# Performance work log

Measured on AMD Instinct MI355X. Metric: run time of the kernel, lower is better.

## Reference

```python
import jax, jax.numpy as jnp
import numpy as np

B, C, W, H = 2, 64, 96, 96  # N = W*H = 9216 spatial positions


def conv1x1(x, w, b):
    # x: (B, Cin, W, H), w: (Cout, Cin), b: (Cout,) -> (B, Cout, W, H)
    return jnp.einsum('bchw,oc->bohw', x, w) + b[None, :, None, None]


def setup_inputs() -> dict:
    key = jax.random.key(0)
    ks = jax.random.split(key, 4)
    c8 = C // 8
    s = 0.05  # small weight scale keeps softmax logits in a sane range
    return {
        'x': jax.random.normal(ks[0], (B, C, W, H), jnp.float32),
        'wq': jax.random.normal(ks[1], (c8, C), jnp.float32) * s,
        'bq': jnp.zeros((c8,), jnp.float32),
        'wk': jax.random.normal(ks[2], (c8, C), jnp.float32) * s,
        'bk': jnp.zeros((c8,), jnp.float32),
        'wv': jax.random.normal(ks[3], (C, C), jnp.float32) * s,
        'bv': jnp.zeros((C,), jnp.float32),
        'gamma': jnp.full((1,), 0.5, jnp.float32),
    }


def reference(x, wq, bq, wk, bk, wv, bv, gamma):
    b, c, w, h = x.shape
    n = w * h
    q = conv1x1(x, wq, bq).reshape(b, -1, n)   # (B, C//8, N)
    k = conv1x1(x, wk, bk).reshape(b, -1, n)   # (B, C//8, N)
    v = conv1x1(x, wv, bv).reshape(b, c, n)    # (B, C, N)
    energy = jnp.einsum('bci,bcj->bij', q, k)  # (B, N, N)
    attn = jax.nn.softmax(energy, axis=-1)
    # torch.bmm(v, attn): out[b,c,i] = sum_j v[b,c,j] * attn[b,j,i]
    out = jnp.einsum('bcj,bji->bci', v, attn).reshape(b, c, w, h)
    return gamma * out + x
```

## Files before the change

kernel.cpp:

```cpp
#include <hip/hip_runtime.h>

using half2v  = __attribute__((ext_vector_type(2))) _Float16;
using half4   = __attribute__((ext_vector_type(4))) _Float16;
using half8   = __attribute__((ext_vector_type(8))) _Float16;
using floatx4 = __attribute__((ext_vector_type(4))) float;

constexpr int BATCH = 2;
constexpr int NPOS  = 96 * 96;
constexpr int NT    = NPOS / 16;
constexpr int NST   = NPOS / 32;

#define EXP2(x) __builtin_amdgcn_exp2f(x)
#define MFMA16(A, B, C) __builtin_amdgcn_mfma_f32_16x16x16f16(A, B, C, 0, 0, 0)
#define MFMA32(A, B, C) __builtin_amdgcn_mfma_f32_16x16x32_f16(A, B, C, 0, 0, 0)

__device__ inline half8 p8_of(floatx4 e0, floatx4 e1) {
    half2v a0 = __builtin_bit_cast(half2v,
        __builtin_amdgcn_cvt_pkrtz(EXP2(e0[0]), EXP2(e0[1])));
    half2v a1 = __builtin_bit_cast(half2v,
        __builtin_amdgcn_cvt_pkrtz(EXP2(e0[2]), EXP2(e0[3])));
    half2v a2 = __builtin_bit_cast(half2v,
        __builtin_amdgcn_cvt_pkrtz(EXP2(e1[0]), EXP2(e1[1])));
    half2v a3 = __builtin_bit_cast(half2v,
        __builtin_amdgcn_cvt_pkrtz(EXP2(e1[2]), EXP2(e1[3])));
    half8 p = {a0[0], a0[1], a1[0], a1[1], a2[0], a2[1], a3[0], a3[1]};
    return p;
}

__global__ __launch_bounds__(256) void qkv_kernel(
    const float* __restrict__ x,
    const float* __restrict__ wq, const float* __restrict__ bq,
    const float* __restrict__ wk, const float* __restrict__ bk,
    const float* __restrict__ wv, const float* __restrict__ bv,
    _Float16* __restrict__ Qf, _Float16* __restrict__ Kf,
    _Float16* __restrict__ Vf)
{
    __shared__ float W[80][64];
    __shared__ float bias[80];
    __shared__ float qs[32][9];
    __shared__ float ks[32][9];
    __shared__ _Float16 vs[32][72];
    const int tid = threadIdx.x;
    for (int idx = tid; idx < 80 * 64; idx += 256) {
        int o = idx >> 6, c = idx & 63;
        float w;
        if (o < 8)       w = wq[o * 64 + c];
        else if (o < 16) w = wk[(o - 8) * 64 + c];
        else             w = wv[(o - 16) * 64 + c];
        W[o][c] = w;
    }
    if (tid < 80) {
        float bb;
        if (tid < 8)       bb = bq[tid];
        else if (tid < 16) bb = bk[tid - 8];
        else               bb = bv[tid - 16];
        bias[tid] = bb;
    }
    __syncthreads();

    const int js = blockIdx.x;
    const int b  = blockIdx.y;
    const int part = tid >> 5;
    const int jl   = tid & 31;
    const int i    = js * 32 + jl;

    float xr[64];
    #pragma unroll
    for (int c = 0; c < 64; ++c)
        xr[c] = x[(size_t)(b * 64 + c) * NPOS + i];

    #pragma unroll
    for (int q = 0; q < 10; ++q) {
        const int o = part * 10 + q;
        float s = bias[o];
        #pragma unroll
        for (int c4 = 0; c4 < 16; ++c4) {
            float4 w4 = *(const float4*)&W[o][c4 * 4];
            s += w4.x * xr[c4*4+0] + w4.y * xr[c4*4+1]
               + w4.z * xr[c4*4+2] + w4.w * xr[c4*4+3];
        }
        if (o < 8)       qs[jl][o] = s;
        else if (o < 16) ks[jl][o - 8] = s;
        else             vs[jl][o - 16] = (_Float16)s;
    }
    __syncthreads();

    const size_t tile = (size_t)b * NST + js;
    {
        const int ct = tid >> 6, l = tid & 63;
        const int g = l >> 4, cl = l & 15;
        half8 o8;
        #pragma unroll
        for (int idx = 0; idx < 8; ++idx)
            o8[idx] = vs[8 * g + idx][16 * ct + cl];
        *(half8*)&Vf[(tile * 256 + ct * 64 + l) * 8] = o8;
    }
    if (tid < 128) {
        const int l = tid >> 1, e = tid & 1;
        const int m = l & 15, g = l >> 4;
        const int jsrc = 8 * (m >> 2) + 4 * e + (m & 3);
        constexpr float LOG2E = 1.44269504088896f;
        half4 qh;
        #pragma unroll
        for (int r = 0; r < 4; ++r)
            qh[r] = (g < 2) ? (_Float16)(qs[jsrc][4 * g + r] * LOG2E)
                            : (_Float16)0.f;
        ((half4*)Qf)[(tile * 64 + l) * 2 + e] = qh;
    } else {
        const int t = tid - 128;
        const int ht = t >> 6, l = t & 63;
        const int il = l & 15, g = l >> 4;
        const int it = js * 2 + ht;
        half4 kh;
        #pragma unroll
        for (int r = 0; r < 4; ++r) {
            if (g < 2)       kh[r] = (_Float16)ks[16 * ht + il][4 * g + r];
            else if (g == 2) kh[r] = (r < 2) ? (_Float16)1.f : (_Float16)0.f;
            else             kh[r] = (_Float16)0.f;
        }
        ((half4*)Kf)[(size_t)(b * NT + it) * 64 + l] = kh;
    }
}

template<int JSPLIT>
__global__ __launch_bounds__(256, 2) void attn_kernel(
    const _Float16* __restrict__ Qf, const _Float16* __restrict__ Kf,
    const _Float16* __restrict__ Vf,
    float* __restrict__ part, float* __restrict__ part_rs)
{
    constexpr int NSTEP = NST / JSPLIT / 4;
    __shared__ half8 P0[4][4][64];
    __shared__ half8 P1[4][4][64];
    __shared__ float rsred[4][4][16];
    const int s   = blockIdx.x;
    const int jh  = blockIdx.y;
    const int b   = s & 1;
    const int igl = s >> 1;
    const int tid = threadIdx.x;
    const int w = tid >> 6, l = tid & 63;
    const int wc = w & 1, wj = w >> 1;
    const int it0 = igl * 4, i0 = igl * 64;

    const half8* __restrict__ qfb = (const half8*)Qf + (size_t)b * NST * 64;
    const half4* __restrict__ kfb = (const half4*)Kf + (size_t)b * NT * 64;
    const half8* __restrict__ vfb = (const half8*)Vf + (size_t)b * NST * 256;

    half4 kf[4];
    #pragma unroll
    for (int st = 0; st < 4; ++st) kf[st] = kfb[(size_t)(it0 + st) * 64 + l];

    half8 vones;
    #pragma unroll
    for (int e = 0; e < 8; ++e)
        vones[e] = (_Float16)(((l & 15) == 0) ? 1.f : 0.f);

    floatx4 acc[4][2];
    floatx4 rs[4];
    #pragma unroll
    for (int st = 0; st < 4; ++st) {
        acc[st][0] = (floatx4){0.f, 0.f, 0.f, 0.f};
        acc[st][1] = (floatx4){0.f, 0.f, 0.f, 0.f};
        rs[st]     = (floatx4){0.f, 0.f, 0.f, 0.f};
    }

    const floatx4 z = {0.f, 0.f, 0.f, 0.f};
    const int st0 = jh * (NST / JSPLIT);

    const half8* qp = qfb + (size_t)(st0 + 8 + w) * 64 + l;
    const half8* vb = vfb + (size_t)(st0 + 2 * wj) * 256 + wc * 128 + l;
    const int o_own  = wc * 256;
    const int o_part = 256 - o_own;

    half8 qA = qfb[(size_t)(st0 + w) * 64 + l];
    half8 qB = qfb[(size_t)(st0 + 4 + w) * 64 + l];
    half8 pwA[4], pwB[4];

    {
        half4 qe0 = __builtin_shufflevector(qA, qA, 0, 1, 2, 3);
        half4 qe1 = __builtin_shufflevector(qA, qA, 4, 5, 6, 7);
        #pragma unroll
        for (int ist = 0; ist < 4; ++ist) {
            floatx4 e0 = MFMA16(qe0, kf[ist], z);
            floatx4 e1 = MFMA16(qe1, kf[ist], z);
            half8 pw = p8_of(e0, e1);
            rs[ist] = MFMA32(vones, pw, rs[ist]);
            P0[w][ist][l] = pw;
            pwA[ist] = pw;
        }
    }
    __syncthreads();

    #define BODY(PRD, PWR, PWOLD, PWNEW, QUSE, QPRE) do { \
        half8 pr0 = PRD[w ^ 1][0][l], pr1 = PRD[w ^ 1][1][l]; \
        half8 pr2 = PRD[w ^ 1][2][l], pr3 = PRD[w ^ 1][3][l]; \
        half8 vo0 = vb[o_own],  vo1 = vb[o_own + 64]; \
        half8 vq0 = vb[o_part], vq1 = vb[o_part + 64]; \
        QPRE = qp[0]; qp += 256; \
        half4 qe0 = __builtin_shufflevector(QUSE, QUSE, 0, 1, 2, 3); \
        half4 qe1 = __builtin_shufflevector(QUSE, QUSE, 4, 5, 6, 7); \
        _Pragma("unroll") \
        for (int ist = 0; ist < 4; ++ist) { \
            floatx4 e0 = MFMA16(qe0, kf[ist], z); \
            floatx4 e1 = MFMA16(qe1, kf[ist], z); \
            half8 pw = p8_of(e0, e1); \
            rs[ist] = MFMA32(vones, pw, rs[ist]); \
            PWR[w][ist][l] = pw; \
            PWNEW[ist] = pw; \
        } \
        _Pragma("unroll") \
        for (int ist = 0; ist < 4; ++ist) { \
            acc[ist][0] = MFMA32(vo0, PWOLD[ist], acc[ist][0]); \
            acc[ist][1] = MFMA32(vo1, PWOLD[ist], acc[ist][1]); \
        } \
        acc[0][0] = MFMA32(vq0, pr0, acc[0][0]); \
        acc[0][1] = MFMA32(vq1, pr0, acc[0][1]); \
        acc[1][0] = MFMA32(vq0, pr1, acc[1][0]); \
        acc[1][1] = MFMA32(vq1, pr1, acc[1][1]); \
        acc[2][0] = MFMA32(vq0, pr2, acc[2][0]); \
        acc[2][1] = MFMA32(vq1, pr2, acc[2][1]); \
        acc[3][0] = MFMA32(vq0, pr3, acc[3][0]); \
        acc[3][1] = MFMA32(vq1, pr3, acc[3][1]); \
        vb += 1024; \
        __syncthreads(); \
    } while (0)

    for (int t = 0; t < (NSTEP - 2) / 2; ++t) {
        BODY(P0, P1, pwA, pwB, qB, qA);
        BODY(P1, P0, pwB, pwA, qA, qB);
    }
    BODY(P0, P1, pwA, pwB, qB, qA);
    #undef BODY

    {
        half8 pr0 = P1[w ^ 1][0][l], pr1 = P1[w ^ 1][1][l];
        half8 pr2 = P1[w ^ 1][2][l], pr3 = P1[w ^ 1][3][l];
        half8 vo0 = vb[o_own],  vo1 = vb[o_own + 64];
        half8 vq0 = vb[o_part], vq1 = vb[o_part + 64];
        #pragma unroll
        for (int ist = 0; ist < 4; ++ist) {
            acc[ist][0] = MFMA32(vo0, pwB[ist], acc[ist][0]);
            acc[ist][1] = MFMA32(vo1, pwB[ist], acc[ist][1]);
        }
        acc[0][0] = MFMA32(vq0, pr0, acc[0][0]);
        acc[0][1] = MFMA32(vq1, pr0, acc[0][1]);
        acc[1][0] = MFMA32(vq0, pr1, acc[1][0]);
        acc[1][1] = MFMA32(vq1, pr1, acc[1][1]);
        acc[2][0] = MFMA32(vq0, pr2, acc[2][0]);
        acc[2][1] = MFMA32(vq1, pr2, acc[2][1]);
        acc[3][0] = MFMA32(vq0, pr3, acc[3][0]);
        acc[3][1] = MFMA32(vq1, pr3, acc[3][1]);
    }
    __syncthreads();

    float4* mrg = (float4*)&P0[0][0][0];
    if (wj == 1) {
        #pragma unroll
        for (int ist = 0; ist < 4; ++ist)
            #pragma unroll
            for (int cti = 0; cti < 2; ++cti)
                mrg[(size_t)((wc * 8 + ist * 2 + cti) * 64) + l] =
                    *(float4*)&acc[ist][cti];
    }
    if (l < 16) {
        #pragma unroll
        for (int ist = 0; ist < 4; ++ist) rsred[w][ist][l] = rs[ist][0];
    }
    __syncthreads();

    float* __restrict__ P  = part    + (size_t)jh * ((size_t)BATCH * 64 * NPOS);
    float* __restrict__ Pr = part_rs + (size_t)jh * ((size_t)BATCH * NPOS);
    if (wj == 0) {
        const int iq = i0 + (l & 15);
        #pragma unroll
        for (int ist = 0; ist < 4; ++ist)
            #pragma unroll
            for (int cti = 0; cti < 2; ++cti) {
                float4 m = mrg[(size_t)((wc * 8 + ist * 2 + cti) * 64) + l];
                float4 a = *(float4*)&acc[ist][cti];
                a.x += m.x; a.y += m.y; a.z += m.z; a.w += m.w;
                #pragma unroll
                for (int r = 0; r < 4; ++r) {
                    int c = 16 * (2 * wc + cti) + 4 * (l >> 4) + r;
                    size_t o = ((size_t)(b * 64 + c)) * NPOS + iq + 16 * ist;
                    P[o] = (&a.x)[r];
                }
            }
    }
    if (w == 0 && l < 16) {
        #pragma unroll
        for (int ist = 0; ist < 4; ++ist) {
            float rsv = rsred[0][ist][l] + rsred[1][ist][l]
                      + rsred[2][ist][l] + rsred[3][ist][l];
            Pr[(size_t)b * NPOS + i0 + 16 * ist + l] = rsv;
        }
    }
}

template<int JSPLIT>
__global__ __launch_bounds__(256) void combine_kernel(
    const float* __restrict__ part, const float* __restrict__ part_rs,
    const float* __restrict__ x, const float* __restrict__ gamma,
    float* __restrict__ out)
{
    const float g = gamma[0];
    const size_t idx = (size_t)blockIdx.x * 256 + threadIdx.x;
    const size_t stride  = ((size_t)BATCH * 64 * NPOS) / 4;
    const size_t rstride = ((size_t)BATCH * NPOS) / 4;
    const int i4 = (int)(idx % (NPOS / 4));
    const int b  = (int)(idx / ((size_t)64 * (NPOS / 4)));
    const float4* p0 = (const float4*)part;
    const float4* r0 = (const float4*)part_rs;

    float4 a = p0[idx];
    float4 rsum = r0[(size_t)b * (NPOS / 4) + i4];
    #pragma unroll
    for (int u = 1; u < JSPLIT; ++u) {
        float4 q = p0[idx + (size_t)u * stride];
        a.x += q.x; a.y += q.y; a.z += q.z; a.w += q.w;
        float4 rq = r0[(size_t)b * (NPOS / 4) + i4 + (size_t)u * rstride];
        rsum.x += rq.x; rsum.y += rq.y; rsum.z += rq.z; rsum.w += rq.w;
    }
    float4 xv = ((const float4*)x)[idx];
    float4 o;
    o.x = g * (a.x / rsum.x) + xv.x;
    o.y = g * (a.y / rsum.y) + xv.y;
    o.z = g * (a.z / rsum.z) + xv.z;
    o.w = g * (a.w / rsum.w) + xv.w;
    ((float4*)out)[idx] = o;
}

extern "C" void kernel_launch(void* const* d_in, const int* in_sizes, int n_in,
                              void* d_out, int out_size, void* d_ws, size_t ws_size,
                              hipStream_t stream)
{
    const float* x     = (const float*)d_in[0];
    const float* wq    = (const float*)d_in[1];
    const float* bq    = (const float*)d_in[2];
    const float* wk    = (const float*)d_in[3];
    const float* bk    = (const float*)d_in[4];
    const float* wv    = (const float*)d_in[5];
    const float* bv    = (const float*)d_in[6];
    const float* gamma = (const float*)d_in[7];
    float* out = (float*)d_out;

    char* wsb = (char*)d_ws;
    _Float16* Qf = (_Float16*)wsb;
    _Float16* Kf = (_Float16*)(wsb + 589824);
    _Float16* Vf = (_Float16*)(wsb + 1179648);
    float*    Pp = (float*)(wsb + 3538944);

    qkv_kernel<<<dim3(NST, BATCH), 256, 0, stream>>>(
        x, wq, bq, wk, bk, wv, bv, Qf, Kf, Vf);

    const size_t partBytes = (size_t)BATCH * 64 * NPOS * sizeof(float);
    const size_t rsBytes   = (size_t)BATCH * NPOS * sizeof(float);
    const size_t need4 = 3538944 + 4 * (partBytes + rsBytes);
    const int nblk = (BATCH * 64 * NPOS / 4) / 256;

    if (ws_size >= need4) {
        float* Prs = (float*)(wsb + 3538944 + 4 * partBytes);
        attn_kernel<4><<<dim3(NST, 4), 256, 0, stream>>>(Qf, Kf, Vf, Pp, Prs);
        combine_kernel<4><<<nblk, 256, 0, stream>>>(Pp, Prs, x, gamma, out);
    } else {
        float* Prs = (float*)(wsb + 3538944 + 2 * partBytes);
        attn_kernel<2><<<dim3(NST, 2), 256, 0, stream>>>(Qf, Kf, Vf, Pp, Prs);
        combine_kernel<2><<<nblk, 256, 0, stream>>>(Pp, Prs, x, gamma, out);
    }
}
```

Before: 123.6 us.

## Double query tile per block to 128 rows and split keys six ways

Each attention block now covers 128 query positions (8 subtiles) instead of 64, so every V fragment loaded from global memory feeds twice as many MFMAs. The own-wave P values are re-read from LDS instead of being held in registers, which frees registers for the larger accumulators. The key dimension is split 6 ways (grid 144x6) to keep enough blocks in flight, at the cost of more partial buffers for the combine pass to read. Register pressure under launch_bounds(256,2) is higher and could cause spills.

```diff
diff --git a/kernel.cpp b/kernel.cpp
--- a/kernel.cpp
+++ b/kernel.cpp
@@ -128,10 +128,10 @@
     const _Float16* __restrict__ Vf,
     float* __restrict__ part, float* __restrict__ part_rs)
 {
-    constexpr int NSTEP = NST / JSPLIT / 4;
-    __shared__ half8 P0[4][4][64];
-    __shared__ half8 P1[4][4][64];
-    __shared__ float rsred[4][4][16];
+    constexpr int NSTEP  = NST / JSPLIT / 4;
+    constexpr int NBODY  = NSTEP - 1;
+    __shared__ half8 P0[4][8][64];
+    __shared__ half8 P1[4][8][64];
     const int s   = blockIdx.x;
     const int jh  = blockIdx.y;
     const int b   = s & 1;
@@ -139,25 +139,25 @@
     const int tid = threadIdx.x;
     const int w = tid >> 6, l = tid & 63;
     const int wc = w & 1, wj = w >> 1;
-    const int it0 = igl * 4, i0 = igl * 64;
+    const int it0 = igl * 8, i0 = igl * 128;
 
     const half8* __restrict__ qfb = (const half8*)Qf + (size_t)b * NST * 64;
     const half4* __restrict__ kfb = (const half4*)Kf + (size_t)b * NT * 64;
     const half8* __restrict__ vfb = (const half8*)Vf + (size_t)b * NST * 256;
 
-    half4 kf[4];
-    #pragma unroll
-    for (int st = 0; st < 4; ++st) kf[st] = kfb[(size_t)(it0 + st) * 64 + l];
+    half4 kf[8];
+    #pragma unroll
+    for (int st = 0; st < 8; ++st) kf[st] = kfb[(size_t)(it0 + st) * 64 + l];
 
     half8 vones;
     #pragma unroll
     for (int e = 0; e < 8; ++e)
         vones[e] = (_Float16)(((l & 15) == 0) ? 1.f : 0.f);
 
-    floatx4 acc[4][2];
-    floatx4 rs[4];
-    #pragma unroll
-    for (int st = 0; st < 4; ++st) {
+    floatx4 acc[8][2];
+    floatx4 rs[8];
+    #pragma unroll
+    for (int st = 0; st < 8; ++st) {
         acc[st][0] = (floatx4){0.f, 0.f, 0.f, 0.f};
         acc[st][1] = (floatx4){0.f, 0.f, 0.f, 0.f};
         rs[st]     = (floatx4){0.f, 0.f, 0.f, 0.f};
@@ -173,97 +173,89 @@
 
     half8 qA = qfb[(size_t)(st0 + w) * 64 + l];
     half8 qB = qfb[(size_t)(st0 + 4 + w) * 64 + l];
-    half8 pwA[4], pwB[4];
 
     {
         half4 qe0 = __builtin_shufflevector(qA, qA, 0, 1, 2, 3);
         half4 qe1 = __builtin_shufflevector(qA, qA, 4, 5, 6, 7);
         #pragma unroll
-        for (int ist = 0; ist < 4; ++ist) {
+        for (int ist = 0; ist < 8; ++ist) {
             floatx4 e0 = MFMA16(qe0, kf[ist], z);
             floatx4 e1 = MFMA16(qe1, kf[ist], z);
             half8 pw = p8_of(e0, e1);
             rs[ist] = MFMA32(vones, pw, rs[ist]);
             P0[w][ist][l] = pw;
-            pwA[ist] = pw;
-        }
-    }
-    __syncthreads();
-
-    #define BODY(PRD, PWR, PWOLD, PWNEW, QUSE, QPRE) do { \
-        half8 pr0 = PRD[w ^ 1][0][l], pr1 = PRD[w ^ 1][1][l]; \
-        half8 pr2 = PRD[w ^ 1][2][l], pr3 = PRD[w ^ 1][3][l]; \
+        }
+    }
+    __syncthreads();
+
+    #define BODY(PRD, PWR, QUSE, QPRE) do { \
         half8 vo0 = vb[o_own],  vo1 = vb[o_own + 64]; \
         half8 vq0 = vb[o_part], vq1 = vb[o_part + 64]; \
         QPRE = qp[0]; qp += 256; \
         half4 qe0 = __builtin_shufflevector(QUSE, QUSE, 0, 1, 2, 3); \
         half4 qe1 = __builtin_shufflevector(QUSE, QUSE, 4, 5, 6, 7); \
         _Pragma("unroll") \
-        for (int ist = 0; ist < 4; ++ist) { \
+        for (int ist = 0; ist < 8; ++ist) { \
             floatx4 e0 = MFMA16(qe0, kf[ist], z); \
             floatx4 e1 = MFMA16(qe1, kf[ist], z); \
             half8 pw = p8_of(e0, e1); \
             rs[ist] = MFMA32(vones, pw, rs[ist]); \
             PWR[w][ist][l] = pw; \
-            PWNEW[ist] = pw; \
         } \
         _Pragma("unroll") \
-        for (int ist = 0; ist < 4; ++ist) { \
-            acc[ist][0] = MFMA32(vo0, PWOLD[ist], acc[ist][0]); \
-            acc[ist][1] = MFMA32(vo1, PWOLD[ist], acc[ist][1]); \
+        for (int ist = 0; ist < 8; ++ist) { \
+            half8 po = PRD[w][ist][l]; \
+            half8 pp = PRD[w ^ 1][ist][l]; \
+            acc[ist][0] = MFMA32(vo0, po, acc[ist][0]); \
+            acc[ist][1] = MFMA32(vo1, po, acc[ist][1]); \
+            acc[ist][0] = MFMA32(vq0, pp, acc[ist][0]); \
+            acc[ist][1] = MFMA32(vq1, pp, acc[ist][1]); \
         } \
-        acc[0][0] = MFMA32(vq0, pr0, acc[0][0]); \
-        acc[0][1] = MFMA32(vq1, pr0, acc[0][1]); \
-        acc[1][0] = MFMA32(vq0, pr1, acc[1][0]); \
-        acc[1][1] = MFMA32(vq1, pr1, acc[1][1]); \
-        acc[2][0] = MFMA32(vq0, pr2, acc[2][0]); \
-        acc[2][1] = MFMA32(vq1, pr2, acc[2][1]); \
-        acc[3][0] = MFMA32(vq0, pr3, acc[3][0]); \
-        acc[3][1] = MFMA32(vq1, pr3, acc[3][1]); \
         vb += 1024; \
         __syncthreads(); \
     } while (0)
 
-    for (int t = 0; t < (NSTEP - 2) / 2; ++t) {
-        BODY(P0, P1, pwA, pwB, qB, qA);
-        BODY(P1, P0, pwB, pwA, qA, qB);
-    }
-    BODY(P0, P1, pwA, pwB, qB, qA);
-    #undef BODY
+    for (int t = 0; t < NBODY / 2; ++t) {
+        BODY(P0, P1, qB, qA);
+        BODY(P1, P0, qA, qB);
+    }
+    if constexpr (NBODY & 1)
+        BODY(P0, P1, qB, qA);
 
     {
-        half8 pr0 = P1[w ^ 1][0][l], pr1 = P1[w ^ 1][1][l];
-        half8 pr2 = P1[w ^ 1][2][l], pr3 = P1[w ^ 1][3][l];
         half8 vo0 = vb[o_own],  vo1 = vb[o_own + 64];
         half8 vq0 = vb[o_part], vq1 = vb[o_part + 64];
         #pragma unroll
-        for (int ist = 0; ist < 4; ++ist) {
-            acc[ist][0] = MFMA32(vo0, pwB[ist], acc[ist][0]);
-            acc[ist][1] = MFMA32(vo1, pwB[ist], acc[ist][1]);
-        }
-        acc[0][0] = MFMA32(vq0, pr0, acc[0][0]);
-        acc[0][1] = MFMA32(vq1, pr0, acc[0][1]);
-        acc[1][0] = MFMA32(vq0, pr1, acc[1][0]);
-        acc[1][1] = MFMA32(vq1, pr1, acc[1][1]);
-        acc[2][0] = MFMA32(vq0, pr2, acc[2][0]);
-        acc[2][1] = MFMA32(vq1, pr2, acc[2][1]);
-        acc[3][0] = MFMA32(vq0, pr3, acc[3][0]);
-        acc[3][1] = MFMA32(vq1, pr3, acc[3][1]);
-    }
-    __syncthreads();
-
-    float4* mrg = (float4*)&P0[0][0][0];
+        for (int ist = 0; ist < 8; ++ist) {
+            half8 po, pp;
+            if constexpr (NBODY & 1) {
+                po = P1[w][ist][l];     pp = P1[w ^ 1][ist][l];
+            } else {
+                po = P0[w][ist][l];     pp = P0[w ^ 1][ist][l];
+            }
+            acc[ist][0] = MFMA32(vo0, po, acc[ist][0]);
+            acc[ist][1] = MFMA32(vo1, po, acc[ist][1]);
+            acc[ist][0] = MFMA32(vq0, pp, acc[ist][0]);
+            acc[ist][1] = MFMA32(vq1, pp, acc[ist][1]);
+        }
+    }
+    #undef BODY
+    __syncthreads();
+
+    float4* mrg   = (float4*)&P0[0][0][0];
+    float*  rsrd  = (float*)&P1[0][0][0];
     if (wj == 1) {
         #pragma unroll
-        for (int ist = 0; ist < 4; ++ist)
+        for (int ist = 0; ist < 8; ++ist)
             #pragma unroll
             for (int cti = 0; cti < 2; ++cti)
-                mrg[(size_t)((wc * 8 + ist * 2 + cti) * 64) + l] =
+                mrg[(size_t)((wc * 16 + ist * 2 + cti) * 64) + l] =
                     *(float4*)&acc[ist][cti];
     }
     if (l < 16) {
         #pragma unroll
-        for (int ist = 0; ist < 4; ++ist) rsred[w][ist][l] = rs[ist][0];
+        for (int ist = 0; ist < 8; ++ist)
+            rsrd[(w * 8 + ist) * 16 + l] = rs[ist][0];
     }
     __syncthreads();
 
@@ -272,10 +264,10 @@
     if (wj == 0) {
         const int iq = i0 + (l & 15);
         #pragma unroll
-        for (int ist = 0; ist < 4; ++ist)
+        for (int ist = 0; ist < 8; ++ist)
             #pragma unroll
             for (int cti = 0; cti < 2; ++cti) {
-                float4 m = mrg[(size_t)((wc * 8 + ist * 2 + cti) * 64) + l];
+                float4 m = mrg[(size_t)((wc * 16 + ist * 2 + cti) * 64) + l];
                 float4 a = *(float4*)&acc[ist][cti];
                 a.x += m.x; a.y += m.y; a.z += m.z; a.w += m.w;
                 #pragma unroll
@@ -288,9 +280,11 @@
     }
     if (w == 0 && l < 16) {
         #pragma unroll
-        for (int ist = 0; ist < 4; ++ist) {
-            float rsv = rsred[0][ist][l] + rsred[1][ist][l]
-                      + rsred[2][ist][l] + rsred[3][ist][l];
+        for (int ist = 0; ist < 8; ++ist) {
+            float rsv = rsrd[(0 * 8 + ist) * 16 + l]
+                      + rsrd[(1 * 8 + ist) * 16 + l]
+                      + rsrd[(2 * 8 + ist) * 16 + l]
+                      + rsrd[(3 * 8 + ist) * 16 + l];
             Pr[(size_t)b * NPOS + i0 + 16 * ist + l] = rsv;
         }
     }
@@ -354,16 +348,16 @@
 
     const size_t partBytes = (size_t)BATCH * 64 * NPOS * sizeof(float);
     const size_t rsBytes   = (size_t)BATCH * NPOS * sizeof(float);
-    const size_t need4 = 3538944 + 4 * (partBytes + rsBytes);
+    const size_t need6 = 3538944 + 6 * (partBytes + rsBytes);
     const int nblk = (BATCH * 64 * NPOS / 4) / 256;
 
-    if (ws_size >= need4) {
+    if (ws_size >= need6) {
+        float* Prs = (float*)(wsb + 3538944 + 6 * partBytes);
+        attn_kernel<6><<<dim3(144, 6), 256, 0, stream>>>(Qf, Kf, Vf, Pp, Prs);
+        combine_kernel<6><<<nblk, 256, 0, stream>>>(Pp, Prs, x, gamma, out);
+    } else {
         float* Prs = (float*)(wsb + 3538944 + 4 * partBytes);
-        attn_kernel<4><<<dim3(NST, 4), 256, 0, stream>>>(Qf, Kf, Vf, Pp, Prs);
+        attn_kernel<4><<<dim3(144, 4), 256, 0, stream>>>(Qf, Kf, Vf, Pp, Prs);
         combine_kernel<4><<<nblk, 256, 0, stream>>>(Pp, Prs, x, gamma, out);
-    } else {
-        float* Prs = (float*)(wsb + 3538944 + 2 * partBytes);
-        attn_kernel<2><<<dim3(NST, 2), 256, 0, stream>>>(Qf, Kf, Vf, Pp, Prs);
-        combine_kernel<2><<<nblk, 256, 0, stream>>>(Pp, Prs, x, gamma, out);
-    }
-}
+    }
+}
```

After: 129.9 us. 1.05x slower.
